# Kernel tuning notes

Hardware: AMD Instinct MI355X
Metric: run time of the kernel (lower is better)

Reference implementation:

```python
import jax, jax.numpy as jnp
import numpy as np

MAX_RANGE = 100.0


def _conv3x3(x, w, b):
    # x: [B,C,H,W], w: [2,C,3,3], b: [2]
    y = jax.lax.conv_general_dilated(
        x, w, window_strides=(1, 1), padding='SAME',
        dimension_numbers=('NCHW', 'OIHW', 'NCHW'))
    return y + b[None, :, None, None]


def setup_inputs() -> dict:
    key = jax.random.key(0)
    k1, k2, k3 = jax.random.split(key, 3)
    B, C, H, W = 4, 64, 64, 64
    x = jax.random.normal(k1, (B, C, H, W), dtype=jnp.float32)
    conv_w = jax.random.normal(k2, (2, C, 3, 3), dtype=jnp.float32) * 0.05
    conv_b = jax.random.normal(k3, (2,), dtype=jnp.float32) * 0.05
    return {'x': x, 'conv_w': conv_w, 'conv_b': conv_b}


def reference(x, conv_w, conv_b):
    # alpha, beta: [B,1,H,W]
    ab = MAX_RANGE * jnp.tanh(_conv3x3(x, conv_w, conv_b))
    alpha, beta = ab[:, 0:1], ab[:, 1:2]

    # Pairwise differences d[b,i,j,h,w] = beta[b]*x[b,i] - x[b,j]  -> [B,C,C,H,W]
    d = beta[:, :, None] * x[:, :, None] - x[:, None, :]
    a = alpha[:, :, None]  # [B,1,1,H,W]

    # softAbs: softmax over the pair {d, -d} weighted by clamped alpha*d logits
    v1 = jnp.clip(d * a, -MAX_RANGE, MAX_RANGE)
    v2 = jnp.clip(-d * a, -MAX_RANGE, MAX_RANGE)
    m = jnp.maximum(v1, v2)
    e1 = jnp.exp(v1 - m)
    e2 = jnp.exp(v2 - m)
    p1 = e1 / (e1 + e2)
    sabs = d * (2.0 * p1 - 1.0)  # d*p1 + (-d)*(1-p1)

    # mean over i (the expand dim) -> [B,C,H,W]
    tmp = jnp.mean(sabs, axis=1)

    # softArgMin over channel dim
    sam = jax.nn.softmax(jnp.clip(-tmp * alpha, -MAX_RANGE, MAX_RANGE), axis=1)

    # soft median, keepdims -> [B,1,H,W]
    return jnp.sum(x * sam, axis=1, keepdims=True)
```

## Files before the change

### kernel.cpp

```cpp
#include <hip/hip_runtime.h>
#include <math.h>

#define MAXR 100.0f
#define LOG2E 1.4426950408889634f

__device__ __forceinline__ float exp2_fast(float x) { return __builtin_amdgcn_exp2f(x); }
__device__ __forceinline__ float rcp_fast(float x)  { return __builtin_amdgcn_rcpf(x); }
__device__ __forceinline__ float bcast_lane(float v, int i) {
    return __int_as_float(__builtin_amdgcn_readlane(__float_as_int(v), i));
}

__device__ __forceinline__ float tanh_fast(float s) {
    float E = exp2_fast(2.0f * LOG2E * fabsf(s));
    float t = fmaf(-2.0f, rcp_fast(E + 1.0f), 1.0f);
    return copysignf(t, s);
}

template<int CTRL>
__device__ __forceinline__ float dpp0(float v) {
    return __int_as_float(__builtin_amdgcn_update_dpp(0, __float_as_int(v), CTRL, 0xf, 0xf, true));
}
template<int CTRL>
__device__ __forceinline__ float dppk(float v) {
    return __int_as_float(__builtin_amdgcn_update_dpp(__float_as_int(v), __float_as_int(v), CTRL, 0xf, 0xf, false));
}
__device__ __forceinline__ float wave_sum(float v) {
    v += dpp0<0x111>(v);
    v += dpp0<0x112>(v);
    v += dpp0<0x114>(v);
    v += dpp0<0x118>(v);
    v += dpp0<0x142>(v);
    v += dpp0<0x143>(v);
    return bcast_lane(v, 63);
}
__device__ __forceinline__ float wave_max(float v) {
    v = fmaxf(v, dppk<0x111>(v));
    v = fmaxf(v, dppk<0x112>(v));
    v = fmaxf(v, dppk<0x114>(v));
    v = fmaxf(v, dppk<0x118>(v));
    v = fmaxf(v, dppk<0x142>(v));
    v = fmaxf(v, dppk<0x143>(v));
    return bcast_lane(v, 63);
}

__global__ __launch_bounds__(256, 4) void dsf_fused(const float* __restrict__ x,
                                                    const float* __restrict__ wg,
                                                    const float* __restrict__ bias,
                                                    float* __restrict__ out) {
    __shared__ float xs[64 * 57];

    const int tid  = threadIdx.x;
    const int lane = tid & 63;
    const int wave = tid >> 6;

    const int p0 = blockIdx.x * 16;
    const int b  = p0 >> 12;
    const int h  = (p0 >> 6) & 63;
    const int w0 = p0 & 63;

    float wr0[9], wr1[9];
    #pragma unroll
    for (int k = 0; k < 9; ++k) {
        wr0[k] = wg[lane * 9 + k];
        wr1[k] = wg[576 + lane * 9 + k];
    }
    const float b0 = bias[0], b1 = bias[1];

    const float* xbase = x + b * 262144;
    for (int e = tid; e < 3456; e += 256) {
        int c   = e / 54;
        int rem = e - c * 54;
        int r   = rem / 18;
        int wt  = rem - r * 18;
        int hh  = h + r - 1;
        int ww  = w0 - 1 + wt;
        float v = 0.f;
        if (hh >= 0 && hh < 64 && (unsigned)ww < 64u)
            v = xbase[c * 4096 + hh * 64 + ww];
        xs[c * 57 + r * 19 + wt] = v;
    }
    __syncthreads();

    const float* xc = xs + lane * 57;
    float win[3][6];
    #pragma unroll
    for (int r = 0; r < 3; ++r)
        #pragma unroll
        for (int t = 0; t < 6; ++t)
            win[r][t] = xc[r * 19 + wave * 4 + t];

    float be[4], aa[4], c2[4], xj[4];
    #pragma unroll
    for (int p = 0; p < 4; ++p) {
        float a0 = 0.f, a1 = 0.f;
        #pragma unroll
        for (int r = 0; r < 3; ++r) {
            #pragma unroll
            for (int t = 0; t < 3; ++t) {
                float xv = win[r][p + t];
                a0 = fmaf(xv, wr0[r * 3 + t], a0);
                a1 = fmaf(xv, wr1[r * 3 + t], a1);
            }
        }
        a0 = wave_sum(a0);
        a1 = wave_sum(a1);
        float al = MAXR * tanh_fast(a0 + b0);
        be[p]    = MAXR * tanh_fast(a1 + b1);
        aa[p]    = fabsf(al);
        c2[p]    = 2.0f * LOG2E * aa[p];
        xj[p]    = win[1][p + 1];
    }

    float A[4] = {0.f, 0.f, 0.f, 0.f};
    #pragma unroll 4
    for (int i = 0; i < 64; ++i) {
        #pragma unroll
        for (int p = 0; p < 4; ++p) {
            float s = bcast_lane(xj[p], i);
            float d = fmaf(be[p], s, -xj[p]);
            float E = exp2_fast(c2[p] * fabsf(d));
            float r = rcp_fast(E + 1.0f);
            float u = fmaf(-2.0f, r, 1.0f);
            A[p] = fmaf(fabsf(d), u, A[p]);
        }
    }

    #pragma unroll
    for (int p = 0; p < 4; ++p) {
        float gl = fmaxf(-A[p] * aa[p] * (1.0f / 64.0f), -MAXR);
        float gm = wave_max(gl);
        float ew = exp2_fast((gl - gm) * LOG2E);
        float den = wave_sum(ew);
        float num = wave_sum(xj[p] * ew);
        if (lane == 0) out[p0 + wave * 4 + p] = num * rcp_fast(den);
    }
}

extern "C" void kernel_launch(void* const* d_in, const int* in_sizes, int n_in,
                              void* d_out, int out_size, void* d_ws, size_t ws_size,
                              hipStream_t stream) {
    const float* x      = (const float*)d_in[0];
    const float* conv_w = (const float*)d_in[1];
    const float* conv_b = (const float*)d_in[2];
    float* out = (float*)d_out;
    (void)d_ws; (void)ws_size;

    dsf_fused<<<1024, 256, 0, stream>>>(x, conv_w, conv_b, out);
}
```

Before: 86.24 us.

## Skip saturated softAbs terms using wave min/max bounds and ballot masks

For each pixel the kernel takes the wave-wide max and min of x and a threshold derived from alpha. It then marks channels i whose beta*x_i lies beyond every x_j by that margin; for those, tanh has saturated and |d|·tanh reduces to a signed linear sum. Those terms are added in closed form with wave sums and popcounts. Only the remaining channels run the exp/rcp loop, iterated over a uniform ballot mask. This removes most of the transcendental work when beta is large. In exchange it serializes the per-pixel loops, losing the four-way interleaving across pixels, and the loop length now depends on the data.

Measured after the change: 74.95 us. -13.1%, faster.

```diff
diff --git a/kernel.cpp b/kernel.cpp
--- a/kernel.cpp
+++ b/kernel.cpp
@@ -40,6 +40,15 @@
     v = fmaxf(v, dppk<0x118>(v));
     v = fmaxf(v, dppk<0x142>(v));
     v = fmaxf(v, dppk<0x143>(v));
+    return bcast_lane(v, 63);
+}
+__device__ __forceinline__ float wave_min(float v) {
+    v = fminf(v, dppk<0x111>(v));
+    v = fminf(v, dppk<0x112>(v));
+    v = fminf(v, dppk<0x114>(v));
+    v = fminf(v, dppk<0x118>(v));
+    v = fminf(v, dppk<0x142>(v));
+    v = fminf(v, dppk<0x143>(v));
     return bcast_lane(v, 63);
 }
 
@@ -111,25 +120,40 @@
         xj[p]    = win[1][p + 1];
     }
 
-    float A[4] = {0.f, 0.f, 0.f, 0.f};
-    #pragma unroll 4
-    for (int i = 0; i < 64; ++i) {
-        #pragma unroll
-        for (int p = 0; p < 4; ++p) {
-            float s = bcast_lane(xj[p], i);
-            float d = fmaf(be[p], s, -xj[p]);
-            float E = exp2_fast(c2[p] * fabsf(d));
-            float r = rcp_fast(E + 1.0f);
-            float u = fmaf(-2.0f, r, 1.0f);
-            A[p] = fmaf(fabsf(d), u, A[p]);
-        }
-    }
-
     #pragma unroll
     for (int p = 0; p < 4; ++p) {
-        float gl = fmaxf(-A[p] * aa[p] * (1.0f / 64.0f), -MAXR);
+        const float M   = wave_max(xj[p]);
+        const float mN  = wave_min(xj[p]);
+        const float thr = 29.0f * rcp_fast(c2[p]);
+        const float bx  = be[p] * xj[p];
+
+        const bool isp = bx >= M + thr;
+        const bool isn = bx <= mN - thr;
+        unsigned long long pm = __ballot(isp);
+        unsigned long long nm = __ballot(isn);
+        unsigned long long hm = ~(pm | nm);
+
+        float SP = wave_sum(isp ? bx : 0.0f);
+        float SN = wave_sum(isn ? bx : 0.0f);
+        int   CP = __popcll(pm);
+        int   CN = __popcll(nm);
+
+        float A = (SP - SN) + (float)(CN - CP) * xj[p];
+
+        while (hm) {
+            int i = __ffsll((long long)hm) - 1;
+            hm &= hm - 1;
+            float s = bcast_lane(xj[p], i);
+            float d = fabsf(fmaf(be[p], s, -xj[p]));
+            float m = c2[p] * d;
+            float E = exp2_fast(m);
+            float r = rcp_fast(E + 1.0f);
+            A = fmaf(d, fmaf(-2.0f, r, 1.0f), A);
+        }
+
+        float gl = fmaxf(-A * aa[p] * (1.0f / 64.0f), -MAXR);
         float gm = wave_max(gl);
-        float ew = exp2_fast((gl - gm) * LOG2E);
+        float ew  = exp2_fast((gl - gm) * LOG2E);
         float den = wave_sum(ew);
         float num = wave_sum(xj[p] * ew);
         if (lane == 0) out[p0 + wave * 4 + p] = num * rcp_fast(den);
```
